# Performance work log

Hardware: AMD Instinct MI355X
Metric: run time of the kernel (lower is better)

## Reference

```python
import jax, jax.numpy as jnp
import numpy as np

B, C, H, W = 4, 256, 48, 48
HEADS, DIM_HEAD, SCALE = 8, 64, 10.0
INNER = HEADS * DIM_HEAD
EPS = 1e-12


def setup_inputs() -> dict:
    key = jax.random.key(0)
    k1, k2, k3, k4 = jax.random.split(key, 4)
    x = jax.random.normal(k1, (B, C, H, W), dtype=jnp.float32)
    # 1x1 conv weights stored as [out_ch, in_ch]
    w_qkv = jax.random.normal(k2, (3 * INNER, C), dtype=jnp.float32) * (1.0 / np.sqrt(C))
    w_out = jax.random.normal(k3, (C, INNER), dtype=jnp.float32) * (1.0 / np.sqrt(INNER))
    b_out = jax.random.normal(k4, (C,), dtype=jnp.float32) * 0.01
    return {"x": x, "w_qkv": w_qkv, "w_out": w_out, "b_out": b_out}


def _l2norm(t):
    # normalize along last axis, clamping the norm at EPS (matches torch l2norm)
    denom = jnp.maximum(jnp.linalg.norm(t, axis=-1, keepdims=True), EPS)
    return t / denom


def reference(x, w_qkv, w_out, b_out):
    b, c, h, w = x.shape
    n = h * w
    # 1x1 conv QKV projection: [B, 3*INNER, H, W]
    qkv = jnp.einsum('oc,bchw->bohw', w_qkv, x)
    q, k, v = jnp.split(qkv, 3, axis=1)
    # [B, heads, dim_head, N] -> [B, heads, N, dim_head]
    def to_bhnd(t):
        return t.reshape(b, HEADS, DIM_HEAD, n).transpose(0, 1, 3, 2)
    q = _l2norm(to_bhnd(q))
    k = _l2norm(to_bhnd(k))
    v = to_bhnd(v)
    sim = jnp.einsum('bhid,bhjd->bhij', q, k) * SCALE  # [B,h,N,N]
    attn = jax.nn.softmax(sim, axis=-1)
    out = jnp.einsum('bhij,bhjd->bhid', attn, v)  # [B,h,N,d]
    # back to [B, INNER, H, W]
    out = out.transpose(0, 1, 3, 2).reshape(b, INNER, h, w)
    # 1x1 conv output projection with bias
    out = jnp.einsum('oc,bchw->bohw', w_out, out) + b_out[None, :, None, None]
    return out
```

## Files before the change

kernel.cpp:

```cpp
#include <hip/hip_runtime.h>

typedef unsigned short u16;
typedef __attribute__((ext_vector_type(8))) short bf16x8;
typedef __attribute__((ext_vector_type(4))) float f32x4;

#define MFMA16(A,B,C) __builtin_amdgcn_mfma_f32_16x16x32_bf16(A,B,C,0,0,0)

#define B_ 4
#define C_ 256
#define N_ 2304
#define HEADS_ 8
#define DH_ 64
#define INNER_ 512
#define SCALE_LOG2E 14.426950408889634f

__device__ __forceinline__ u16 f2bf(float f) {
    union { float f; unsigned int u; } v; v.f = f;
    unsigned int r = v.u + 0x7fffu + ((v.u >> 16) & 1u);
    return (u16)(r >> 16);
}
__device__ __forceinline__ unsigned int pk2(float a, float b) {
    union { float f; unsigned int u; } va, vb; va.f = a; vb.f = b;
    return __builtin_amdgcn_perm(vb.u + 0x8000u, va.u + 0x8000u, 0x07060302u);
}

__global__ __launch_bounds__(256) void k_prep(const float* __restrict__ x,
                                              u16* __restrict__ xT,
                                              const float* __restrict__ w_qkv,
                                              u16* __restrict__ wqb,
                                              const float* __restrict__ w_out,
                                              u16* __restrict__ wob) {
    __shared__ float tile[64][65];
    int idx = blockIdx.x;
    int t = threadIdx.x;
    if (idx < 576) {
        int b = idx / 144, rem = idx % 144;
        int n0 = (rem >> 2) * 64, c0 = (rem & 3) * 64;
        const float* xb = x + (size_t)b * C_ * N_;
        u16* xTb = xT + (size_t)b * N_ * C_;
        int r = t >> 4;
        int q4 = (t & 15) * 4;
#pragma unroll
        for (int pass = 0; pass < 4; ++pass) {
            int c = r + pass * 16;
            float4 v = *(const float4*)(xb + (size_t)(c0 + c) * N_ + n0 + q4);
            tile[c][q4+0] = v.x; tile[c][q4+1] = v.y; tile[c][q4+2] = v.z; tile[c][q4+3] = v.w;
        }
        __syncthreads();
#pragma unroll
        for (int pass = 0; pass < 4; ++pass) {
            int n = r + pass * 16;
            ushort4 o;
            o.x = f2bf(tile[q4+0][n]); o.y = f2bf(tile[q4+1][n]);
            o.z = f2bf(tile[q4+2][n]); o.w = f2bf(tile[q4+3][n]);
            *(ushort4*)(xTb + (size_t)(n0 + n) * C_ + c0 + q4) = o;
        }
    } else if (idx < 960) {
        int i = (idx - 576) * 256 + t;
        float4 v = ((const float4*)w_qkv)[i];
        ushort4 o;
        o.x = f2bf(v.x); o.y = f2bf(v.y); o.z = f2bf(v.z); o.w = f2bf(v.w);
        ((ushort4*)wqb)[i] = o;
    } else {
        int i = (idx - 960) * 256 + t;
        float4 v = ((const float4*)w_out)[i];
        ushort4 o;
        o.x = f2bf(v.x); o.y = f2bf(v.y); o.z = f2bf(v.z); o.w = f2bf(v.w);
        ((ushort4*)wob)[i] = o;
    }
}

__global__ __launch_bounds__(256) void k_qkv(const u16* __restrict__ w_qkv,
                                             const u16* __restrict__ xT,
                                             u16* __restrict__ Qn,
                                             u16* __restrict__ Kn,
                                             u16* __restrict__ Vt) {
    __shared__ __align__(16) u16 Wt[64][264];
    __shared__ __align__(16) u16 Xt[64][264];
    int mt = blockIdx.x, nt = blockIdx.y, b = blockIdx.z;
    int tid = threadIdx.x;
    int wv = tid >> 6, lane = tid & 63;
    int col = lane & 15, quad = lane >> 4;
    int o0 = mt * 64;
    const u16* wtile = w_qkv + (size_t)o0 * C_;
    const u16* xtile = xT + ((size_t)b * N_ + nt*64) * C_;
#pragma unroll
    for (int p = 0; p < 8; ++p) {
        int c = p * 256 + tid;
        int row = c >> 5, seg = c & 31;
        *(uint4*)(&Wt[row][seg*8]) = *(const uint4*)(wtile + (size_t)row * C_ + seg*8);
        *(uint4*)(&Xt[row][seg*8]) = *(const uint4*)(xtile + (size_t)row * C_ + seg*8);
    }
    __syncthreads();
    f32x4 z = {0.f, 0.f, 0.f, 0.f};
    f32x4 acc[4]; acc[0]=z; acc[1]=z; acc[2]=z; acc[3]=z;
#pragma unroll
    for (int ks = 0; ks < 8; ++ks) {
        bf16x8 bfrag = *(const bf16x8*)(&Xt[wv*16 + col][ks*32 + quad*8]);
#pragma unroll
        for (int mb = 0; mb < 4; ++mb) {
            bf16x8 afrag = *(const bf16x8*)(&Wt[mb*16 + col][ks*32 + quad*8]);
            acc[mb] = MFMA16(afrag, bfrag, acc[mb]);
        }
    }
    int n = nt * 64 + wv * 16 + col;
    int which = mt >> 3, h = mt & 7;
    if (which < 2) {
        float s = 0.f;
#pragma unroll
        for (int mb = 0; mb < 4; ++mb)
#pragma unroll
            for (int r = 0; r < 4; ++r) s += acc[mb][r] * acc[mb][r];
        s += __shfl_xor(s, 16);
        s += __shfl_xor(s, 32);
        float inv = 1.f / fmaxf(sqrtf(s), 1e-12f);
        u16* dst = (which == 0 ? Qn : Kn) + (((size_t)b * HEADS_ + h) * N_ + n) * DH_;
#pragma unroll
        for (int mb = 0; mb < 4; ++mb) {
            ushort4 o;
            o.x = f2bf(acc[mb][0] * inv); o.y = f2bf(acc[mb][1] * inv);
            o.z = f2bf(acc[mb][2] * inv); o.w = f2bf(acc[mb][3] * inv);
            *(ushort4*)(dst + mb*16 + quad*4) = o;
        }
    } else {
        u16* dst = Vt + ((size_t)b * HEADS_ + h) * (size_t)DH_ * N_;
#pragma unroll
        for (int mb = 0; mb < 4; ++mb)
#pragma unroll
            for (int r = 0; r < 4; ++r)
                dst[(size_t)(mb*16 + quad*4 + r) * N_ + n] = f2bf(acc[mb][r]);
    }
}

__global__ __launch_bounds__(256) void k_attn(const u16* __restrict__ Qn,
                                              const u16* __restrict__ Kn,
                                              const u16* __restrict__ Vt,
                                              u16* __restrict__ AO) {
    __shared__ __align__(16) u16 Kt[64][72];
    __shared__ __align__(16) u16 Vtl[64][72];
    __shared__ __align__(16) u16 plds[4][32][72];
    int head_lin = blockIdx.x & 31;
    int qt = blockIdx.x >> 5;
    int b = head_lin >> 3, h = head_lin & 7;
    int tid = threadIdx.x;
    int wv = tid >> 6, lane = tid & 63;
    int col = lane & 15, quad = lane >> 4;
    size_t head = (size_t)b * HEADS_ + h;
    const u16* Qh = Qn + head * (size_t)N_ * DH_;
    const u16* Kh = Kn + head * (size_t)N_ * DH_;
    const u16* Vh = Vt + head * (size_t)DH_ * N_;
    int q0 = qt * 128 + wv * 32;
    bf16x8 qfA0 = *(const bf16x8*)(Qh + (size_t)(q0 + col) * DH_ + quad*8);
    bf16x8 qfA1 = *(const bf16x8*)(Qh + (size_t)(q0 + col) * DH_ + 32 + quad*8);
    bf16x8 qfB0 = *(const bf16x8*)(Qh + (size_t)(q0 + 16 + col) * DH_ + quad*8);
    bf16x8 qfB1 = *(const bf16x8*)(Qh + (size_t)(q0 + 16 + col) * DH_ + 32 + quad*8);
    f32x4 z = {0.f, 0.f, 0.f, 0.f};
    f32x4 OA[4], OB[4];
#pragma unroll
    for (int i = 0; i < 4; ++i) { OA[i] = z; OB[i] = z; }
    float lA = 0.f, lB = 0.f;
    int srow = tid >> 3, sseg = tid & 7;
    const u16* ksrc0 = Kh + (size_t)tid * 8;
    const u16* vsrc0 = Vh + (size_t)srow * N_ + sseg * 8;

    uint4 k0 = *(const uint4*)(ksrc0);
    uint4 k1 = *(const uint4*)(ksrc0 + 2048);
    uint4 v0 = *(const uint4*)(vsrc0);
    uint4 v1 = *(const uint4*)(vsrc0 + (size_t)32 * N_);

    for (int kt = 0; kt < N_/64; ++kt) {
        *(uint4*)(&Kt[srow][sseg*8])      = k0;
        *(uint4*)(&Kt[32 + srow][sseg*8]) = k1;
        *(uint4*)(&Vtl[srow][sseg*8])      = v0;
        *(uint4*)(&Vtl[32 + srow][sseg*8]) = v1;
        __syncthreads();
        int ktn = kt + 1 < N_/64 ? kt + 1 : kt;
        k0 = *(const uint4*)(ksrc0 + (size_t)ktn * 4096);
        k1 = *(const uint4*)(ksrc0 + (size_t)ktn * 4096 + 2048);
        v0 = *(const uint4*)(vsrc0 + ktn * 64);
        v1 = *(const uint4*)(vsrc0 + (size_t)32 * N_ + ktn * 64);
        float rsA = 0.f, rsB = 0.f;
#pragma unroll
        for (int nb = 0; nb < 4; ++nb) {
            bf16x8 kf0 = *(const bf16x8*)(&Kt[nb*16 + col][quad*8]);
            bf16x8 kf1 = *(const bf16x8*)(&Kt[nb*16 + col][32 + quad*8]);
            f32x4 a = MFMA16(kf0, qfA0, z);
            a = MFMA16(kf1, qfA1, a);
            f32x4 c = MFMA16(kf0, qfB0, z);
            c = MFMA16(kf1, qfB1, c);
            float a0 = exp2f(fmaf(a[0], SCALE_LOG2E, -SCALE_LOG2E));
            float a1 = exp2f(fmaf(a[1], SCALE_LOG2E, -SCALE_LOG2E));
            float a2 = exp2f(fmaf(a[2], SCALE_LOG2E, -SCALE_LOG2E));
            float a3 = exp2f(fmaf(a[3], SCALE_LOG2E, -SCALE_LOG2E));
            float c0 = exp2f(fmaf(c[0], SCALE_LOG2E, -SCALE_LOG2E));
            float c1 = exp2f(fmaf(c[1], SCALE_LOG2E, -SCALE_LOG2E));
            float c2 = exp2f(fmaf(c[2], SCALE_LOG2E, -SCALE_LOG2E));
            float c3 = exp2f(fmaf(c[3], SCALE_LOG2E, -SCALE_LOG2E));
            rsA += (a0 + a1) + (a2 + a3);
            rsB += (c0 + c1) + (c2 + c3);
            uint2 wA, wB;
            wA.x = pk2(a0, a1); wA.y = pk2(a2, a3);
            wB.x = pk2(c0, c1); wB.y = pk2(c2, c3);
            *(uint2*)(&plds[wv][col][nb*16 + quad*4]) = wA;
            *(uint2*)(&plds[wv][16 + col][nb*16 + quad*4]) = wB;
        }
        lA += rsA; lB += rsB;
        __asm__ volatile("" ::: "memory");
#pragma unroll
        for (int ks = 0; ks < 2; ++ks) {
            bf16x8 pfA = *(const bf16x8*)(&plds[wv][col][ks*32 + quad*8]);
            bf16x8 pfB = *(const bf16x8*)(&plds[wv][16 + col][ks*32 + quad*8]);
#pragma unroll
            for (int nb = 0; nb < 4; ++nb) {
                bf16x8 vf = *(const bf16x8*)(&Vtl[nb*16 + col][ks*32 + quad*8]);
                OA[nb] = MFMA16(vf, pfA, OA[nb]);
                OB[nb] = MFMA16(vf, pfB, OB[nb]);
            }
        }
        __asm__ volatile("" ::: "memory");
        __syncthreads();
    }
    lA += __shfl_xor(lA, 16); lA += __shfl_xor(lA, 32);
    lB += __shfl_xor(lB, 16); lB += __shfl_xor(lB, 32);
    float linvA = 1.f / lA, linvB = 1.f / lB;
    u16* dstA = AO + ((size_t)b * N_ + q0 + col) * INNER_ + h * DH_;
    u16* dstB = AO + ((size_t)b * N_ + q0 + 16 + col) * INNER_ + h * DH_;
#pragma unroll
    for (int nb = 0; nb < 4; ++nb) {
        uint2 wA, wB;
        wA.x = pk2(OA[nb][0] * linvA, OA[nb][1] * linvA);
        wA.y = pk2(OA[nb][2] * linvA, OA[nb][3] * linvA);
        wB.x = pk2(OB[nb][0] * linvB, OB[nb][1] * linvB);
        wB.y = pk2(OB[nb][2] * linvB, OB[nb][3] * linvB);
        *(uint2*)(dstA + nb*16 + quad*4) = wA;
        *(uint2*)(dstB + nb*16 + quad*4) = wB;
    }
}

__global__ __launch_bounds__(256) void k_proj(const u16* __restrict__ w_out,
                                              const float* __restrict__ b_out,
                                              const u16* __restrict__ AO,
                                              float* __restrict__ out) {
    __shared__ __align__(16) u16 Wt[64][264];
    __shared__ __align__(16) u16 At[64][264];
    int mt = blockIdx.x, nt = blockIdx.y, b = blockIdx.z;
    int tid = threadIdx.x;
    int wv = tid >> 6, lane = tid & 63;
    int col = lane & 15, quad = lane >> 4;
    int o0b = mt * 64;
    const u16* wtile = w_out + (size_t)o0b * INNER_;
    const u16* atile = AO + ((size_t)b * N_ + nt*64) * INNER_;
    f32x4 z = {0.f, 0.f, 0.f, 0.f};
    f32x4 acc[4]; acc[0]=z; acc[1]=z; acc[2]=z; acc[3]=z;
#pragma unroll
    for (int half = 0; half < 2; ++half) {
        if (half) __syncthreads();
#pragma unroll
        for (int p = 0; p < 8; ++p) {
            int c = p * 256 + tid;
            int row = c >> 5, seg = c & 31;
            *(uint4*)(&Wt[row][seg*8]) =
                *(const uint4*)(wtile + (size_t)row * INNER_ + half*256 + seg*8);
            *(uint4*)(&At[row][seg*8]) =
                *(const uint4*)(atile + (size_t)row * INNER_ + half*256 + seg*8);
        }
        __syncthreads();
#pragma unroll
        for (int ks = 0; ks < 8; ++ks) {
            bf16x8 af = *(const bf16x8*)(&Wt[wv*16 + col][ks*32 + quad*8]);
#pragma unroll
            for (int nb = 0; nb < 4; ++nb) {
                bf16x8 bfv = *(const bf16x8*)(&At[nb*16 + col][ks*32 + quad*8]);
                acc[nb] = MFMA16(af, bfv, acc[nb]);
            }
        }
    }
    int o0 = o0b + wv * 16;
    float bias[4];
#pragma unroll
    for (int r = 0; r < 4; ++r) bias[r] = b_out[o0 + quad*4 + r];
    float* dst = out + ((size_t)b * C_ + o0) * N_ + nt*64;
#pragma unroll
    for (int nb = 0; nb < 4; ++nb)
#pragma unroll
        for (int r = 0; r < 4; ++r)
            dst[(size_t)(quad*4 + r) * N_ + nb*16 + col] = acc[nb][r] + bias[r];
}

extern "C" void kernel_launch(void* const* d_in, const int* in_sizes, int n_in,
                              void* d_out, int out_size, void* d_ws, size_t ws_size,
                              hipStream_t stream) {
    const float* x     = (const float*)d_in[0];
    const float* w_qkv = (const float*)d_in[1];
    const float* w_out = (const float*)d_in[2];
    const float* b_out = (const float*)d_in[3];
    float* out = (float*)d_out;

    char* ws = (char*)d_ws;
    u16* xT  = (u16*)(ws);
    u16* Qn  = (u16*)(ws + 4718592);
    u16* Kn  = (u16*)(ws + 14155776);
    u16* Vt  = (u16*)(ws + 23592960);
    u16* AO  = (u16*)(ws + 33030144);
    u16* wqb = (u16*)(ws + 42467328);
    u16* wob = (u16*)(ws + 43253760);

    hipLaunchKernelGGL(k_prep, dim3(1088), dim3(256), 0, stream, x, xT, w_qkv, wqb, w_out, wob);
    hipLaunchKernelGGL(k_qkv,  dim3(24, N_/64, B_), dim3(256), 0, stream, wqb, xT, Qn, Kn, Vt);
    hipLaunchKernelGGL(k_attn, dim3((N_/128) * 32), dim3(256), 0, stream, Qn, Kn, Vt, AO);
    hipLaunchKernelGGL(k_proj, dim3(C_/64, N_/64, B_), dim3(256), 0, stream, wob, b_out, AO, out);
}
```

Before: 205.2 us.

## Split attention over two key halves with a separate combine kernel

Adds a split-K attention kernel that handles each key/value half in a separate block, doubling the grid from 576 to 1152 blocks so the GPU's compute units are better occupied. It writes unnormalized fp32 partial outputs and row sums to workspace. A combine kernel then sums the halves, normalizes, and converts to bf16. This costs extra fp32 global traffic (about 38 MB written and read back) and one more launch. The split path only runs when the workspace is large enough, otherwise the original kernel is used. It relies on the fixed max (scale) offset because q and k are L2-normalized, so no running max is needed.

Measured after the change: 196.3 us. 1.05x faster.

```diff
diff --git a/kernel.cpp b/kernel.cpp
--- a/kernel.cpp
+++ b/kernel.cpp
@@ -130,6 +130,135 @@
             for (int r = 0; r < 4; ++r)
                 dst[(size_t)(mb*16 + quad*4 + r) * N_ + n] = f2bf(acc[mb][r]);
     }
+}
+
+__global__ __launch_bounds__(256) void k_attn_split(const u16* __restrict__ Qn,
+                                                    const u16* __restrict__ Kn,
+                                                    const u16* __restrict__ Vt,
+                                                    float* __restrict__ Op,
+                                                    float* __restrict__ lp) {
+    __shared__ __align__(16) u16 Kt[64][72];
+    __shared__ __align__(16) u16 Vtl[64][72];
+    __shared__ __align__(16) u16 plds[4][32][72];
+    int head_lin = blockIdx.x & 31;
+    int rest = blockIdx.x >> 5;
+    int qt = rest % 18;
+    int khalf = rest / 18;
+    int b = head_lin >> 3, h = head_lin & 7;
+    int tid = threadIdx.x;
+    int wv = tid >> 6, lane = tid & 63;
+    int col = lane & 15, quad = lane >> 4;
+    size_t head = (size_t)b * HEADS_ + h;
+    const u16* Qh = Qn + head * (size_t)N_ * DH_;
+    const u16* Kh = Kn + head * (size_t)N_ * DH_ + (size_t)khalf * 1152 * DH_;
+    const u16* Vh = Vt + head * (size_t)DH_ * N_;
+    int q0 = qt * 128 + wv * 32;
+    bf16x8 qfA0 = *(const bf16x8*)(Qh + (size_t)(q0 + col) * DH_ + quad*8);
+    bf16x8 qfA1 = *(const bf16x8*)(Qh + (size_t)(q0 + col) * DH_ + 32 + quad*8);
+    bf16x8 qfB0 = *(const bf16x8*)(Qh + (size_t)(q0 + 16 + col) * DH_ + quad*8);
+    bf16x8 qfB1 = *(const bf16x8*)(Qh + (size_t)(q0 + 16 + col) * DH_ + 32 + quad*8);
+    f32x4 z = {0.f, 0.f, 0.f, 0.f};
+    f32x4 OA[4], OB[4];
+#pragma unroll
+    for (int i = 0; i < 4; ++i) { OA[i] = z; OB[i] = z; }
+    float lA = 0.f, lB = 0.f;
+    int srow = tid >> 3, sseg = tid & 7;
+    const u16* ksrc0 = Kh + (size_t)tid * 8;
+    const u16* vsrc0 = Vh + (size_t)srow * N_ + khalf * 1152 + sseg * 8;
+
+    uint4 k0 = *(const uint4*)(ksrc0);
+    uint4 k1 = *(const uint4*)(ksrc0 + 2048);
+    uint4 v0 = *(const uint4*)(vsrc0);
+    uint4 v1 = *(const uint4*)(vsrc0 + (size_t)32 * N_);
+
+    for (int kt = 0; kt < 18; ++kt) {
+        *(uint4*)(&Kt[srow][sseg*8])      = k0;
+        *(uint4*)(&Kt[32 + srow][sseg*8]) = k1;
+        *(uint4*)(&Vtl[srow][sseg*8])      = v0;
+        *(uint4*)(&Vtl[32 + srow][sseg*8]) = v1;
+        __syncthreads();
+        int ktn = kt + 1 < 18 ? kt + 1 : kt;
+        k0 = *(const uint4*)(ksrc0 + (size_t)ktn * 4096);
+        k1 = *(const uint4*)(ksrc0 + (size_t)ktn * 4096 + 2048);
+        v0 = *(const uint4*)(vsrc0 + ktn * 64);
+        v1 = *(const uint4*)(vsrc0 + (size_t)32 * N_ + ktn * 64);
+        float rsA = 0.f, rsB = 0.f;
+#pragma unroll
+        for (int nb = 0; nb < 4; ++nb) {
+            bf16x8 kf0 = *(const bf16x8*)(&Kt[nb*16 + col][quad*8]);
+            bf16x8 kf1 = *(const bf16x8*)(&Kt[nb*16 + col][32 + quad*8]);
+            f32x4 a = MFMA16(kf0, qfA0, z);
+            a = MFMA16(kf1, qfA1, a);
+            f32x4 c = MFMA16(kf0, qfB0, z);
+            c = MFMA16(kf1, qfB1, c);
+            float a0 = exp2f(fmaf(a[0], SCALE_LOG2E, -SCALE_LOG2E));
+            float a1 = exp2f(fmaf(a[1], SCALE_LOG2E, -SCALE_LOG2E));
+            float a2 = exp2f(fmaf(a[2], SCALE_LOG2E, -SCALE_LOG2E));
+            float a3 = exp2f(fmaf(a[3], SCALE_LOG2E, -SCALE_LOG2E));
+            float c0 = exp2f(fmaf(c[0], SCALE_LOG2E, -SCALE_LOG2E));
+            float c1 = exp2f(fmaf(c[1], SCALE_LOG2E, -SCALE_LOG2E));
+            float c2 = exp2f(fmaf(c[2], SCALE_LOG2E, -SCALE_LOG2E));
+            float c3 = exp2f(fmaf(c[3], SCALE_LOG2E, -SCALE_LOG2E));
+            rsA += (a0 + a1) + (a2 + a3);
+            rsB += (c0 + c1) + (c2 + c3);
+            uint2 wA, wB;
+            wA.x = pk2(a0, a1); wA.y = pk2(a2, a3);
+            wB.x = pk2(c0, c1); wB.y = pk2(c2, c3);
+            *(uint2*)(&plds[wv][col][nb*16 + quad*4]) = wA;
+            *(uint2*)(&plds[wv][16 + col][nb*16 + quad*4]) = wB;
+        }
+        lA += rsA; lB += rsB;
+        __asm__ volatile("" ::: "memory");
+#pragma unroll
+        for (int ks = 0; ks < 2; ++ks) {
+            bf16x8 pfA = *(const bf16x8*)(&plds[wv][col][ks*32 + quad*8]);
+            bf16x8 pfB = *(const bf16x8*)(&plds[wv][16 + col][ks*32 + quad*8]);
+#pragma unroll
+            for (int nb = 0; nb < 4; ++nb) {
+                bf16x8 vf = *(const bf16x8*)(&Vtl[nb*16 + col][ks*32 + quad*8]);
+                OA[nb] = MFMA16(vf, pfA, OA[nb]);
+                OB[nb] = MFMA16(vf, pfB, OB[nb]);
+            }
+        }
+        __asm__ volatile("" ::: "memory");
+        __syncthreads();
+    }
+    lA += __shfl_xor(lA, 16); lA += __shfl_xor(lA, 32);
+    lB += __shfl_xor(lB, 16); lB += __shfl_xor(lB, 32);
+    float* dstA = Op + (((size_t)khalf * B_ + b) * N_ + q0 + col) * INNER_ + h * DH_;
+    float* dstB = dstA + (size_t)16 * INNER_;
+#pragma unroll
+    for (int nb = 0; nb < 4; ++nb) {
+        *(f32x4*)(dstA + nb*16 + quad*4) = OA[nb];
+        *(f32x4*)(dstB + nb*16 + quad*4) = OB[nb];
+    }
+    if (quad == 0) {
+        size_t lbase = (((size_t)khalf * B_ + b) * HEADS_ + h) * N_;
+        lp[lbase + q0 + col] = lA;
+        lp[lbase + q0 + 16 + col] = lB;
+    }
+}
+
+__global__ __launch_bounds__(256) void k_comb(const float* __restrict__ Op,
+                                              const float* __restrict__ lp,
+                                              u16* __restrict__ AO) {
+    int g = blockIdx.x * 256 + threadIdx.x;
+    int b = g / 294912;
+    int rem = g % 294912;
+    int n = rem >> 7;
+    int i4 = rem & 127;
+    int h = i4 >> 4;
+    float4 a = ((const float4*)Op)[g];
+    float4 c = ((const float4*)Op)[g + 1179648];
+    float l = lp[((size_t)b * HEADS_ + h) * N_ + n] +
+              lp[(((size_t)B_ + b) * HEADS_ + h) * N_ + n];
+    float inv = 1.f / l;
+    ushort4 o;
+    o.x = f2bf((a.x + c.x) * inv);
+    o.y = f2bf((a.y + c.y) * inv);
+    o.z = f2bf((a.z + c.z) * inv);
+    o.w = f2bf((a.w + c.w) * inv);
+    ((ushort4*)AO)[g] = o;
 }
 
 __global__ __launch_bounds__(256) void k_attn(const u16* __restrict__ Qn,
@@ -304,9 +433,17 @@
     u16* AO  = (u16*)(ws + 33030144);
     u16* wqb = (u16*)(ws + 42467328);
     u16* wob = (u16*)(ws + 43253760);
+    float* Op = (float*)(ws + 43515904);
+    float* lp = (float*)(ws + 81264640);
+    const size_t need = 81854464;
 
     hipLaunchKernelGGL(k_prep, dim3(1088), dim3(256), 0, stream, x, xT, w_qkv, wqb, w_out, wob);
     hipLaunchKernelGGL(k_qkv,  dim3(24, N_/64, B_), dim3(256), 0, stream, wqb, xT, Qn, Kn, Vt);
-    hipLaunchKernelGGL(k_attn, dim3((N_/128) * 32), dim3(256), 0, stream, Qn, Kn, Vt, AO);
+    if (ws_size >= need) {
+        hipLaunchKernelGGL(k_attn_split, dim3(1152), dim3(256), 0, stream, Qn, Kn, Vt, Op, lp);
+        hipLaunchKernelGGL(k_comb, dim3(4608), dim3(256), 0, stream, Op, lp, AO);
+    } else {
+        hipLaunchKernelGGL(k_attn, dim3((N_/128) * 32), dim3(256), 0, stream, Qn, Kn, Vt, AO);
+    }
     hipLaunchKernelGGL(k_proj, dim3(C_/64, N_/64, B_), dim3(256), 0, stream, wob, b_out, AO, out);
 }
```
